# Performance work log

Measured on AMD Instinct MI355X. Metric: run time of the kernel, lower is better.

## Reference

```python
import jax, jax.numpy as jnp
import numpy as np

B, T, V, D = 2048, 32, 1024, 256


def setup_inputs() -> dict:
    key = jax.random.key(0)
    k1, k2 = jax.random.split(key)
    input = jax.random.normal(k1, (B, T, D), dtype=jnp.float32)
    codebook = jax.random.normal(k2, (T, V, D), dtype=jnp.float32)
    return {"input": input, "codebook": codebook}


def reference(input, codebook):
    # input: [B, T, D]; codebook: [T, V, D]
    x = jnp.moveaxis(input, 1, 0)  # [T, B, D]
    # Squared euclidean distances; argmin is invariant to the sqrt in cdist.
    x2 = jnp.sum(x * x, axis=-1)[..., None]            # [T, B, 1]
    c2 = jnp.sum(codebook * codebook, axis=-1)[:, None, :]  # [T, 1, V]
    xc = jnp.einsum('tbd,tvd->tbv', x, codebook)       # [T, B, V]
    d2 = x2 - 2.0 * xc + c2                            # [T, B, V]
    idxes_ = jnp.argmin(d2, axis=-1)                   # [T, B]
    idxes = idxes_.T                                   # [B, T]
    # Direct per-token gather: embed[b, t] = codebook[t, idxes[b, t]]
    embed_ = codebook[jnp.arange(T)[:, None], idxes_]  # [T, B, D]
    embed = jnp.moveaxis(embed_, 0, 1)                 # [B, T, D]
    return embed, idxes
```

## Files before the change

kernel.cpp:

```cpp
#include <hip/hip_runtime.h>
#include <hip/hip_bf16.h>


#define B_ 2048
#define T_ 32
#define V_ 1024
#define D_ 256
#define BT 128
#define VT 128
#define NVT 8
#define CAND_MAX 1280
#define MARGIN 8.0f

typedef __attribute__((ext_vector_type(8))) short short8;
typedef __attribute__((ext_vector_type(4))) float f32x4;

__device__ __forceinline__ unsigned short f2bf(float f) {
    unsigned u = __builtin_bit_cast(unsigned, f);
    unsigned r = u + 0x7FFFu + ((u >> 16) & 1u);
    return (unsigned short)(r >> 16);
}

__device__ __forceinline__ short8 pack8(float4 a, float4 b) {
    short8 r;
    r[0] = (short)f2bf(a.x); r[1] = (short)f2bf(a.y);
    r[2] = (short)f2bf(a.z); r[3] = (short)f2bf(a.w);
    r[4] = (short)f2bf(b.x); r[5] = (short)f2bf(b.y);
    r[6] = (short)f2bf(b.z); r[7] = (short)f2bf(b.w);
    return r;
}

__device__ __forceinline__ void load_lds16(const void* g, void* l) {
    __builtin_amdgcn_global_load_lds(
        (const __attribute__((address_space(1))) unsigned int*)g,
        (__attribute__((address_space(3))) unsigned int*)l, 16, 0, 0);
}

__global__ void prep_kernel(const float* __restrict__ cb, float* __restrict__ c2,
                            unsigned short* __restrict__ cbs) {
    const int wave = threadIdx.x >> 6, lane = threadIdx.x & 63;
    const int row = blockIdx.x * 4 + wave;
    const float4 v4 = *(const float4*)(cb + (size_t)row * D_ + lane * 4);
    float s = v4.x * v4.x + v4.y * v4.y + v4.z * v4.z + v4.w * v4.w;
    #pragma unroll
    for (int off = 32; off; off >>= 1) s += __shfl_down(s, off, 64);
    if (lane == 0) c2[row] = s;

    ushort4 b4;
    b4.x = f2bf(v4.x); b4.y = f2bf(v4.y); b4.z = f2bf(v4.z); b4.w = f2bf(v4.w);
    const int t = row >> 10, v = row & 1023, vt = v >> 7, r7 = v & 127;
    const int kc = lane >> 3, g = (lane >> 1) & 3, half = lane & 1;
    const size_t off_us = ((size_t)((t * NVT + vt) * 8 + kc)) * 4096
                        + (size_t)(r7 * 4 + (g ^ (r7 & 3))) * 8 + half * 4;
    *(ushort4*)(cbs + off_us) = b4;
}

__global__ void c2_kernel(const float* __restrict__ cb, float* __restrict__ c2) {
    const int row = blockIdx.x * 4 + (threadIdx.x >> 6);
    const int lane = threadIdx.x & 63;
    const float4 v = ((const float4*)(cb + (size_t)row * D_))[lane];
    float s = v.x * v.x + v.y * v.y + v.z * v.z + v.w * v.w;
    #pragma unroll
    for (int off = 32; off; off >>= 1) s += __shfl_down(s, off, 64);
    if (lane == 0) c2[row] = s;
}

__global__ __launch_bounds__(256, 2)
void vq_kernel(const float* __restrict__ x, const float* __restrict__ cb,
               const float* __restrict__ c2, const unsigned short* __restrict__ cbs,
               float* __restrict__ out, int use_swz) {
    const int t  = blockIdx.x;
    const int b0 = blockIdx.y * BT;

    __shared__ short8 A_lds[4096];
    __shared__ short8 B_lds[512];
    __shared__ float  minPart[BT * 2];
    __shared__ unsigned long long result[BT];
    __shared__ unsigned s_cand[CAND_MAX];
    __shared__ unsigned s_cnt;

    const int tid = threadIdx.x;
    const int wave = tid >> 6, lane = tid & 63;
    const int wm = wave & 1, wn = wave >> 1;
    const int q = lane >> 4, ln = lane & 15;

    if (tid < BT) result[tid] = ~0ULL;
    minPart[tid] = 3.4e38f;
    if (tid == 0) s_cnt = 0;

    #pragma unroll
    for (int i = 0; i < 16; ++i) {
        int gid = i * 256 + tid, r = gid >> 5, g = gid & 31;
        const float4* src = (const float4*)(x + (((size_t)(b0 + r)) * T_ + t) * D_ + g * 8);
        A_lds[r * 32 + (g ^ (r & 15))] = pack8(src[0], src[1]);
    }

    auto stage_B = [&](int vt, int kc) {
        if (use_swz) {
            const unsigned short* tile = cbs + ((size_t)((t * NVT + vt) * 8 + kc)) * 4096;
            #pragma unroll
            for (int i = 0; i < 2; ++i) {
                const int gr = wave * 128 + i * 64;
                load_lds16(tile + (size_t)(gr + lane) * 8, (void*)(B_lds + gr));
            }
        } else {
            #pragma unroll
            for (int i = 0; i < 2; ++i) {
                int gid = i * 256 + tid, r = gid >> 2, g = gid & 3;
                const float4* src = (const float4*)(cb + ((size_t)t * V_ + vt * VT + r) * D_ + kc * 32 + g * 8);
                B_lds[r * 4 + (g ^ (r & 3))] = pack8(src[0], src[1]);
            }
        }
    };

    stage_B(0, 0);
    __syncthreads();

    for (int vt = 0; vt < NVT; ++vt) {
        f32x4 acc[4][4];
        #pragma unroll
        for (int mt = 0; mt < 4; ++mt)
            #pragma unroll
            for (int nt = 0; nt < 4; ++nt) acc[mt][nt] = (f32x4){0.f, 0.f, 0.f, 0.f};

        for (int kc = 0; kc < 8; ++kc) {
            short8 af[4], bfr[4];
            #pragma unroll
            for (int mt = 0; mt < 4; ++mt) {
                int m = wm * 64 + mt * 16 + ln;
                af[mt] = A_lds[m * 32 + ((kc * 4 + q) ^ ln)];
            }
            #pragma unroll
            for (int nt = 0; nt < 4; ++nt) {
                int n = wn * 64 + nt * 16 + ln;
                bfr[nt] = B_lds[n * 4 + (q ^ (n & 3))];
            }
            __syncthreads();
            if (!(vt == NVT - 1 && kc == 7)) {
                int nk = kc + 1, nv = vt;
                if (nk == 8) { nk = 0; nv = vt + 1; }
                stage_B(nv, nk);
            }
            #pragma unroll
            for (int mt = 0; mt < 4; ++mt)
                #pragma unroll
                for (int nt = 0; nt < 4; ++nt)
                    acc[mt][nt] = __builtin_amdgcn_mfma_f32_16x16x32_bf16(af[mt], bfr[nt], acc[mt][nt], 0, 0, 0);
            __syncthreads();
        }

        const float* c2p = c2 + t * V_ + vt * VT + wn * 64 + ln;
        float cc[4];
        #pragma unroll
        for (int nt = 0; nt < 4; ++nt) cc[nt] = c2p[nt * 16];

        #pragma unroll
        for (int mt = 0; mt < 4; ++mt)
            #pragma unroll
            for (int i = 0; i < 4; ++i) {
                float mn = 3.4e38f;
                #pragma unroll
                for (int nt = 0; nt < 4; ++nt)
                    mn = fminf(mn, fmaf(-2.0f, acc[mt][nt][i], cc[nt]));
                mn = fminf(mn, __shfl_xor(mn, 1, 64));
                mn = fminf(mn, __shfl_xor(mn, 2, 64));
                mn = fminf(mn, __shfl_xor(mn, 4, 64));
                mn = fminf(mn, __shfl_xor(mn, 8, 64));
                if (ln == 0) {
                    int r = wm * 64 + mt * 16 + q * 4 + i;
                    minPart[r * 2 + wn] = fminf(minPart[r * 2 + wn], mn);
                }
            }
        __syncthreads();

        #pragma unroll
        for (int mt = 0; mt < 4; ++mt)
            #pragma unroll
            for (int i = 0; i < 4; ++i) {
                int r = wm * 64 + mt * 16 + q * 4 + i;
                float2 mp = *(const float2*)&minPart[r * 2];
                float thr = fminf(mp.x, mp.y) + MARGIN;
                #pragma unroll
                for (int nt = 0; nt < 4; ++nt) {
                    float s = fmaf(-2.0f, acc[mt][nt][i], cc[nt]);
                    if (s < thr) {
                        int v = vt * VT + wn * 64 + nt * 16 + ln;
                        unsigned pos = atomicAdd(&s_cnt, 1u);
                        if (pos < CAND_MAX) s_cand[pos] = (unsigned)((r << 10) | v);
                    }
                }
            }
    }

    __syncthreads();
    const unsigned ncand = min(s_cnt, (unsigned)CAND_MAX);
    const int grp = tid >> 4, l16 = tid & 15;
    for (unsigned ci = grp; ci < ncand; ci += 16) {
        const unsigned e = s_cand[ci];
        const int row = e >> 10, v = e & 1023;
        const float* xr = x + (((size_t)(b0 + row)) * T_ + t) * D_ + l16 * 16;
        const float* cr = cb + ((size_t)t * V_ + v) * D_ + l16 * 16;
        float dot = 0.f;
        #pragma unroll
        for (int j = 0; j < 4; ++j) {
            float4 a = *(const float4*)(xr + j * 4);
            float4 b = *(const float4*)(cr + j * 4);
            dot = fmaf(a.x, b.x, dot); dot = fmaf(a.y, b.y, dot);
            dot = fmaf(a.z, b.z, dot); dot = fmaf(a.w, b.w, dot);
        }
        dot += __shfl_xor(dot, 1, 64);
        dot += __shfl_xor(dot, 2, 64);
        dot += __shfl_xor(dot, 4, 64);
        dot += __shfl_xor(dot, 8, 64);
        if (l16 == 0) {
            float sc = fmaf(-2.0f, dot, c2[t * V_ + v]);
            unsigned u = __builtin_bit_cast(unsigned, sc);
            u = (u & 0x80000000u) ? ~u : (u | 0x80000000u);
            atomicMin(&result[row], ((unsigned long long)u << 32) | (unsigned)v);
        }
    }
    __syncthreads();

    if (tid < BT)
        out[(size_t)B_ * T_ * D_ + (size_t)(b0 + tid) * T_ + t] =
            (float)(int)(result[tid] & 1023u);

    const int w = tid >> 6, gl = tid & 63;
    #pragma unroll
    for (int i = 0; i < 32; ++i) {
        const int row = w * 32 + i;
        const int idx = (int)(result[row] & 1023u);
        const float4 src = *(const float4*)(cb + ((size_t)t * V_ + idx) * D_ + gl * 4);
        *(float4*)(out + (((size_t)(b0 + row)) * T_ + t) * D_ + gl * 4) = src;
    }
}

extern "C" void kernel_launch(void* const* d_in, const int* in_sizes, int n_in,
                              void* d_out, int out_size, void* d_ws, size_t ws_size,
                              hipStream_t stream) {
    const float* x  = (const float*)d_in[0];
    const float* cb = (const float*)d_in[1];
    float* out = (float*)d_out;
    float* c2  = (float*)d_ws;
    unsigned short* cbs = (unsigned short*)((char*)d_ws + 131072);
    const size_t NEED = 131072 + (size_t)T_ * V_ * D_ * 2;
    const int use_swz = (ws_size >= NEED) ? 1 : 0;

    if (use_swz) prep_kernel<<<dim3(T_ * V_ / 4), 256, 0, stream>>>(cb, c2, cbs);
    else         c2_kernel<<<dim3(T_ * V_ / 4), 256, 0, stream>>>(cb, c2);
    vq_kernel<<<dim3(T_, B_ / BT), 256, 0, stream>>>(x, cb, c2, cbs, out, use_swz);
}
```

Before: 281.9 us.

## Keep codebook fragments in registers and drop LDS staging of B tiles

The codebook tile is no longer staged through LDS with a barrier per k-chunk. Each wave now loads a 64-column slab of bf16 codebook fragments (pre-laid out in MFMA fragment order by a rewritten prep kernel) straight into registers, then sweeps all 128 rows of A from LDS. The per-row running minimum becomes per-wave and barrier-free, and the candidate buffer grows to absorb the looser thresholds that follow. This removes most __syncthreads and the B-tile LDS traffic, at the cost of heavy register pressure (32 short8 per lane), possible lower occupancy, and more candidates to re-check in fp32.

```diff
diff --git a/kernel.cpp b/kernel.cpp
--- a/kernel.cpp
+++ b/kernel.cpp
@@ -7,9 +7,7 @@
 #define V_ 1024
 #define D_ 256
 #define BT 128
-#define VT 128
-#define NVT 8
-#define CAND_MAX 1280
+#define CAND_MAX 2048
 #define MARGIN 8.0f
 
 typedef __attribute__((ext_vector_type(8))) short short8;
@@ -30,29 +28,29 @@
     return r;
 }
 
-__device__ __forceinline__ void load_lds16(const void* g, void* l) {
-    __builtin_amdgcn_global_load_lds(
-        (const __attribute__((address_space(1))) unsigned int*)g,
-        (__attribute__((address_space(3))) unsigned int*)l, 16, 0, 0);
-}
-
 __global__ void prep_kernel(const float* __restrict__ cb, float* __restrict__ c2,
                             unsigned short* __restrict__ cbs) {
-    const int wave = threadIdx.x >> 6, lane = threadIdx.x & 63;
-    const int row = blockIdx.x * 4 + wave;
-    const float4 v4 = *(const float4*)(cb + (size_t)row * D_ + lane * 4);
-    float s = v4.x * v4.x + v4.y * v4.y + v4.z * v4.z + v4.w * v4.w;
-    #pragma unroll
-    for (int off = 32; off; off >>= 1) s += __shfl_down(s, off, 64);
-    if (lane == 0) c2[row] = s;
-
-    ushort4 b4;
-    b4.x = f2bf(v4.x); b4.y = f2bf(v4.y); b4.z = f2bf(v4.z); b4.w = f2bf(v4.w);
-    const int t = row >> 10, v = row & 1023, vt = v >> 7, r7 = v & 127;
-    const int kc = lane >> 3, g = (lane >> 1) & 3, half = lane & 1;
-    const size_t off_us = ((size_t)((t * NVT + vt) * 8 + kc)) * 4096
-                        + (size_t)(r7 * 4 + (g ^ (r7 & 3))) * 8 + half * 4;
-    *(ushort4*)(cbs + off_us) = b4;
+    const int t = blockIdx.x >> 6, cg = blockIdx.x & 63;
+    __shared__ float c2p[4][16];
+    const int tid = threadIdx.x, wave = tid >> 6, lane = tid & 63;
+    float part = 0.f;
+    short8* outp = (short8*)cbs + (size_t)(t * 64 + cg) * 512;
+    #pragma unroll
+    for (int j = 0; j < 2; ++j) {
+        const int lin = tid + j * 256;
+        const int kc = lin >> 6, qq = (lin >> 4) & 3, l = lin & 15;
+        const float* src = cb + ((size_t)t * V_ + cg * 16 + l) * D_ + kc * 32 + qq * 8;
+        const float4 a = ((const float4*)src)[0], b = ((const float4*)src)[1];
+        part += a.x*a.x + a.y*a.y + a.z*a.z + a.w*a.w
+              + b.x*b.x + b.y*b.y + b.z*b.z + b.w*b.w;
+        outp[lin] = pack8(a, b);
+    }
+    part += __shfl_xor(part, 16, 64);
+    part += __shfl_xor(part, 32, 64);
+    if (lane < 16) c2p[wave][lane] = part;
+    __syncthreads();
+    if (tid < 16)
+        c2[t * V_ + cg * 16 + tid] = c2p[0][tid] + c2p[1][tid] + c2p[2][tid] + c2p[3][tid];
 }
 
 __global__ void c2_kernel(const float* __restrict__ cb, float* __restrict__ c2) {
@@ -73,19 +71,17 @@
     const int b0 = blockIdx.y * BT;
 
     __shared__ short8 A_lds[4096];
-    __shared__ short8 B_lds[512];
-    __shared__ float  minPart[BT * 2];
+    __shared__ float  minW[BT * 4];
     __shared__ unsigned long long result[BT];
     __shared__ unsigned s_cand[CAND_MAX];
     __shared__ unsigned s_cnt;
 
     const int tid = threadIdx.x;
     const int wave = tid >> 6, lane = tid & 63;
-    const int wm = wave & 1, wn = wave >> 1;
     const int q = lane >> 4, ln = lane & 15;
 
     if (tid < BT) result[tid] = ~0ULL;
-    minPart[tid] = 3.4e38f;
+    minW[tid] = 3.4e38f; minW[tid + 256] = 3.4e38f;
     if (tid == 0) s_cnt = 0;
 
     #pragma unroll
@@ -94,102 +90,83 @@
         const float4* src = (const float4*)(x + (((size_t)(b0 + r)) * T_ + t) * D_ + g * 8);
         A_lds[r * 32 + (g ^ (r & 15))] = pack8(src[0], src[1]);
     }
-
-    auto stage_B = [&](int vt, int kc) {
+    __syncthreads();
+
+    for (int vp = 0; vp < 4; ++vp) {
+        short8 breg[4][8];
         if (use_swz) {
-            const unsigned short* tile = cbs + ((size_t)((t * NVT + vt) * 8 + kc)) * 4096;
-            #pragma unroll
-            for (int i = 0; i < 2; ++i) {
-                const int gr = wave * 128 + i * 64;
-                load_lds16(tile + (size_t)(gr + lane) * 8, (void*)(B_lds + gr));
+            const short8* bp = (const short8*)cbs
+                + (size_t)(t * 64 + vp * 16 + wave * 4) * 512 + lane;
+            #pragma unroll
+            for (int nt = 0; nt < 4; ++nt)
+                #pragma unroll
+                for (int kc = 0; kc < 8; ++kc)
+                    breg[nt][kc] = bp[nt * 512 + kc * 64];
+        } else {
+            #pragma unroll
+            for (int nt = 0; nt < 4; ++nt) {
+                const int col = vp * 256 + wave * 64 + nt * 16 + ln;
+                const float* cp = cb + ((size_t)t * V_ + col) * D_ + q * 8;
+                #pragma unroll
+                for (int kc = 0; kc < 8; ++kc) {
+                    const float4 a = ((const float4*)(cp + kc * 32))[0];
+                    const float4 b = ((const float4*)(cp + kc * 32))[1];
+                    breg[nt][kc] = pack8(a, b);
+                }
             }
-        } else {
-            #pragma unroll
-            for (int i = 0; i < 2; ++i) {
-                int gid = i * 256 + tid, r = gid >> 2, g = gid & 3;
-                const float4* src = (const float4*)(cb + ((size_t)t * V_ + vt * VT + r) * D_ + kc * 32 + g * 8);
-                B_lds[r * 4 + (g ^ (r & 3))] = pack8(src[0], src[1]);
-            }
-        }
-    };
-
-    stage_B(0, 0);
-    __syncthreads();
-
-    for (int vt = 0; vt < NVT; ++vt) {
-        f32x4 acc[4][4];
-        #pragma unroll
-        for (int mt = 0; mt < 4; ++mt)
-            #pragma unroll
-            for (int nt = 0; nt < 4; ++nt) acc[mt][nt] = (f32x4){0.f, 0.f, 0.f, 0.f};
-
-        for (int kc = 0; kc < 8; ++kc) {
-            short8 af[4], bfr[4];
-            #pragma unroll
-            for (int mt = 0; mt < 4; ++mt) {
-                int m = wm * 64 + mt * 16 + ln;
-                af[mt] = A_lds[m * 32 + ((kc * 4 + q) ^ ln)];
-            }
-            #pragma unroll
-            for (int nt = 0; nt < 4; ++nt) {
-                int n = wn * 64 + nt * 16 + ln;
-                bfr[nt] = B_lds[n * 4 + (q ^ (n & 3))];
-            }
-            __syncthreads();
-            if (!(vt == NVT - 1 && kc == 7)) {
-                int nk = kc + 1, nv = vt;
-                if (nk == 8) { nk = 0; nv = vt + 1; }
-                stage_B(nv, nk);
-            }
-            #pragma unroll
-            for (int mt = 0; mt < 4; ++mt)
-                #pragma unroll
-                for (int nt = 0; nt < 4; ++nt)
-                    acc[mt][nt] = __builtin_amdgcn_mfma_f32_16x16x32_bf16(af[mt], bfr[nt], acc[mt][nt], 0, 0, 0);
-            __syncthreads();
-        }
-
-        const float* c2p = c2 + t * V_ + vt * VT + wn * 64 + ln;
+        }
         float cc[4];
         #pragma unroll
-        for (int nt = 0; nt < 4; ++nt) cc[nt] = c2p[nt * 16];
-
-        #pragma unroll
-        for (int mt = 0; mt < 4; ++mt)
+        for (int nt = 0; nt < 4; ++nt)
+            cc[nt] = c2[t * V_ + vp * 256 + wave * 64 + nt * 16 + ln];
+
+        #pragma unroll 1
+        for (int mt = 0; mt < 8; ++mt) {
+            f32x4 acc[4];
+            #pragma unroll
+            for (int nt = 0; nt < 4; ++nt) acc[nt] = (f32x4){0.f, 0.f, 0.f, 0.f};
+            #pragma unroll
+            for (int kh = 0; kh < 2; ++kh) {
+                short8 af[4];
+                #pragma unroll
+                for (int j2 = 0; j2 < 4; ++j2) {
+                    const int kc = kh * 4 + j2;
+                    af[j2] = A_lds[(mt * 16 + ln) * 32 + ((kc * 4 + q) ^ ln)];
+                }
+                #pragma unroll
+                for (int j2 = 0; j2 < 4; ++j2)
+                    #pragma unroll
+                    for (int nt = 0; nt < 4; ++nt)
+                        acc[nt] = __builtin_amdgcn_mfma_f32_16x16x32_bf16(
+                            af[j2], breg[nt][kh * 4 + j2], acc[nt], 0, 0, 0);
+            }
+            float s[4][4];
+            #pragma unroll
+            for (int nt = 0; nt < 4; ++nt)
+                #pragma unroll
+                for (int i = 0; i < 4; ++i)
+                    s[nt][i] = fmaf(-2.0f, acc[nt][i], cc[nt]);
             #pragma unroll
             for (int i = 0; i < 4; ++i) {
-                float mn = 3.4e38f;
-                #pragma unroll
-                for (int nt = 0; nt < 4; ++nt)
-                    mn = fminf(mn, fmaf(-2.0f, acc[mt][nt][i], cc[nt]));
+                float mn = fminf(fminf(s[0][i], s[1][i]), fminf(s[2][i], s[3][i]));
                 mn = fminf(mn, __shfl_xor(mn, 1, 64));
                 mn = fminf(mn, __shfl_xor(mn, 2, 64));
                 mn = fminf(mn, __shfl_xor(mn, 4, 64));
                 mn = fminf(mn, __shfl_xor(mn, 8, 64));
-                if (ln == 0) {
-                    int r = wm * 64 + mt * 16 + q * 4 + i;
-                    minPart[r * 2 + wn] = fminf(minPart[r * 2 + wn], mn);
-                }
-            }
-        __syncthreads();
-
-        #pragma unroll
-        for (int mt = 0; mt < 4; ++mt)
-            #pragma unroll
-            for (int i = 0; i < 4; ++i) {
-                int r = wm * 64 + mt * 16 + q * 4 + i;
-                float2 mp = *(const float2*)&minPart[r * 2];
-                float thr = fminf(mp.x, mp.y) + MARGIN;
+                const int row = mt * 16 + q * 4 + i;
+                const float old = minW[row * 4 + wave];
+                const float thr = fminf(old, mn) + MARGIN;
                 #pragma unroll
                 for (int nt = 0; nt < 4; ++nt) {
-                    float s = fmaf(-2.0f, acc[mt][nt][i], cc[nt]);
-                    if (s < thr) {
-                        int v = vt * VT + wn * 64 + nt * 16 + ln;
-                        unsigned pos = atomicAdd(&s_cnt, 1u);
-                        if (pos < CAND_MAX) s_cand[pos] = (unsigned)((r << 10) | v);
+                    if (s[nt][i] < thr) {
+                        const int v = vp * 256 + wave * 64 + nt * 16 + ln;
+                        const unsigned pos = atomicAdd(&s_cnt, 1u);
+                        if (pos < CAND_MAX) s_cand[pos] = (unsigned)((row << 10) | v);
                     }
                 }
+                if (ln == 0) minW[row * 4 + wave] = fminf(old, mn);
             }
+        }
     }
 
     __syncthreads();
@@ -225,13 +202,12 @@
         out[(size_t)B_ * T_ * D_ + (size_t)(b0 + tid) * T_ + t] =
             (float)(int)(result[tid] & 1023u);
 
-    const int w = tid >> 6, gl = tid & 63;
     #pragma unroll
     for (int i = 0; i < 32; ++i) {
-        const int row = w * 32 + i;
+        const int row = wave * 32 + i;
         const int idx = (int)(result[row] & 1023u);
-        const float4 src = *(const float4*)(cb + ((size_t)t * V_ + idx) * D_ + gl * 4);
-        *(float4*)(out + (((size_t)(b0 + row)) * T_ + t) * D_ + gl * 4) = src;
+        const float4 src = *(const float4*)(cb + ((size_t)t * V_ + idx) * D_ + lane * 4);
+        *(float4*)(out + (((size_t)(b0 + row)) * T_ + t) * D_ + lane * 4) = src;
     }
 }
 
@@ -246,7 +222,7 @@
     const size_t NEED = 131072 + (size_t)T_ * V_ * D_ * 2;
     const int use_swz = (ws_size >= NEED) ? 1 : 0;
 
-    if (use_swz) prep_kernel<<<dim3(T_ * V_ / 4), 256, 0, stream>>>(cb, c2, cbs);
+    if (use_swz) prep_kernel<<<dim3(T_ * V_ / 16), 256, 0, stream>>>(cb, c2, cbs);
     else         c2_kernel<<<dim3(T_ * V_ / 4), 256, 0, stream>>>(cb, c2);
     vq_kernel<<<dim3(T_, B_ / BT), 256, 0, stream>>>(x, cb, c2, cbs, out, use_swz);
 }
```

New measurement: 336.9 us. 19.5% more time.
